# Performance work log

Hardware: AMD Instinct MI355X
Metric: run time of the kernel (lower is better)

Reference implementation:

```python
import jax, jax.numpy as jnp
import numpy as np

N, E, DIN, H, DOUT, G = 100000, 1600000, 32, 64, 8, 64
NUM_PROC = 2
EDGE_DIM = 15


def setup_inputs() -> dict:
    key = jax.random.key(0)
    ks = jax.random.split(key, 20)
    s = 0.1
    return {
        "x": jax.random.normal(ks[0], (N, DIN), dtype=jnp.float32),
        "edge_index": jax.random.randint(ks[1], (2, E), 0, N, dtype=jnp.int32),
        "edge_attr": jax.random.normal(ks[2], (E, EDGE_DIM), dtype=jnp.float32),
        "batch": jnp.sort(jax.random.randint(ks[3], (N,), 0, G, dtype=jnp.int32)),
        "enc_W": jax.random.normal(ks[4], (DIN, H)) * s,
        "enc_b": jnp.zeros((H,), jnp.float32),
        "lin_W": jax.random.normal(ks[5], (NUM_PROC, H, H)) * s,
        "lin_b": jnp.zeros((NUM_PROC, H), jnp.float32),
        "edge_W": jax.random.normal(ks[6], (NUM_PROC, EDGE_DIM, H)) * s,
        "edge_b": jnp.zeros((NUM_PROC, H), jnp.float32),
        "att_W1": jax.random.normal(ks[7], (H, H // 2)) * s,
        "att_b1": jnp.zeros((H // 2,), jnp.float32),
        "att_W2": jax.random.normal(ks[8], (H // 2, 1)) * s,
        "att_b2": jnp.zeros((1,), jnp.float32),
        "dec_W1": jax.random.normal(ks[9], (H, H // 2)) * s,
        "dec_b1": jnp.zeros((H // 2,), jnp.float32),
        "dec_W2": jax.random.normal(ks[10], (H // 2, DOUT)) * s,
        "dec_b2": jnp.zeros((DOUT,), jnp.float32),
    }


def reference(x, edge_index, edge_attr, batch, enc_W, enc_b, lin_W, lin_b,
              edge_W, edge_b, att_W1, att_b1, att_W2, att_b2,
              dec_W1, dec_b1, dec_W2, dec_b2):
    src, dst = edge_index[0], edge_index[1]
    n = x.shape[0]
    # encoder
    h = jax.nn.relu(x @ enc_W + enc_b)
    # message passing layers: gather x_j -> linear + edge embedding -> scatter-add
    for l in range(NUM_PROC):
        msg = h[src] @ lin_W[l] + lin_b[l] + edge_attr @ edge_W[l] + edge_b[l]  # [E, H]
        h = jax.nn.relu(jax.ops.segment_sum(msg, dst, num_segments=n))
    # attention global pooling: segment softmax over graphs in `batch`
    scores = (jax.nn.relu(h @ att_W1 + att_b1) @ att_W2 + att_b2)[:, 0]  # [N]
    m = jax.ops.segment_max(scores, batch, num_segments=G)
    e = jnp.exp(scores - m[batch])
    denom = jax.ops.segment_sum(e, batch, num_segments=G)
    attn = e / denom[batch]
    g = jax.ops.segment_sum(h * attn[:, None], batch, num_segments=G)  # [G, H]
    # decoder
    return jax.nn.relu(g @ dec_W1 + dec_b1) @ dec_W2 + dec_b2
```

## Files before the change

### kernel.cpp

```cpp
#include <hip/hip_runtime.h>

#define DIN 32
#define HDIM 64
#define DOUT 8
#define NGRAPH 64
#define EDIM 15
#define SCAN_BS 512

__device__ __forceinline__ int clampidx(int v, int n) {
    return ((unsigned)v < (unsigned)n) ? v : 0;
}

__device__ __forceinline__ unsigned short f2b(float f) {
    unsigned int u = __float_as_uint(f);
    u = (u + 0x7FFF + ((u >> 16) & 1)) >> 16;
    return (unsigned short)u;
}
__device__ __forceinline__ float b2f(unsigned short b) {
    return __uint_as_float(((unsigned int)b) << 16);
}

__global__ __launch_bounds__(256) void k_zero(float* __restrict__ p, size_t n) {
    size_t i = (size_t)blockIdx.x * blockDim.x + threadIdx.x;
    const size_t stride = (size_t)gridDim.x * blockDim.x;
    for (; i < n; i += stride) p[i] = 0.f;
}

__global__ __launch_bounds__(256) void k_enc_b(const float* __restrict__ x,
                                               const float* __restrict__ W,
                                               const float* __restrict__ b,
                                               unsigned short* __restrict__ h, int n_nodes) {
    __shared__ float xs[4][DIN];
    const int j = threadIdx.x & 63;
    const int q = threadIdx.x >> 6;
    const int n = blockIdx.x * 4 + q;
    const bool ok = (n < n_nodes);
    if (ok && j < DIN) xs[q][j] = x[(size_t)n * DIN + j];
    __syncthreads();
    if (ok) {
        float acc = b[j];
#pragma unroll
        for (int k = 0; k < DIN; ++k) acc = fmaf(xs[q][k], W[k * HDIM + j], acc);
        h[(size_t)n * HDIM + j] = f2b(fmaxf(acc, 0.f));
    }
}

__global__ __launch_bounds__(256) void k_deg(const int* __restrict__ ei,
                                             int* __restrict__ degi,
                                             int* __restrict__ rank, int E, int n_nodes) {
    int e = blockIdx.x * blockDim.x + threadIdx.x;
    if (e < E) rank[e] = atomicAdd(&degi[clampidx(ei[E + e], n_nodes)], 1);
}

__global__ __launch_bounds__(SCAN_BS) void k_blocksum(const int* __restrict__ degi,
                                                      int* __restrict__ bsum, int n) {
    __shared__ int red[SCAN_BS];
    const int t = threadIdx.x;
    const int i = blockIdx.x * SCAN_BS + t;
    red[t] = (i < n) ? degi[i] : 0;
    __syncthreads();
    for (int off = SCAN_BS / 2; off >= 1; off >>= 1) {
        if (t < off) red[t] += red[t + off];
        __syncthreads();
    }
    if (t == 0) bsum[blockIdx.x] = red[0];
}

__global__ __launch_bounds__(64) void k_bscan(const int* __restrict__ bsum,
                                              int* __restrict__ boff,
                                              int* __restrict__ offsets,
                                              int nblk, int n, int E) {
    if (blockIdx.x == 0 && threadIdx.x == 0) {
        int run = 0;
        for (int b = 0; b < nblk; ++b) { boff[b] = run; run += bsum[b]; }
        offsets[n] = E;
    }
}

__global__ __launch_bounds__(64) void k_fillofs(const int* __restrict__ degi,
                                                const int* __restrict__ boff,
                                                int* __restrict__ offsets, int n) {
    if (threadIdx.x != 0) return;
    const int b = blockIdx.x;
    int run = boff[b];
    const int i0 = b * SCAN_BS;
    const int i1 = (i0 + SCAN_BS < n) ? i0 + SCAN_BS : n;
    for (int i = i0; i < i1; ++i) {
        offsets[i] = run;
        run += degi[i];
    }
}

__global__ __launch_bounds__(256) void k_fill(const int* __restrict__ ei,
                                              const int* __restrict__ offsets,
                                              const int* __restrict__ rank,
                                              int2* __restrict__ pe, int E, int n_nodes) {
    int e = blockIdx.x * blockDim.x + threadIdx.x;
    if (e >= E) return;
    int dst = clampidx(ei[E + e], n_nodes);
    int pos = offsets[dst] + rank[e];
    if ((unsigned)pos < (unsigned)E) pe[pos] = make_int2(clampidx(ei[e], n_nodes), e);
}

__global__ __launch_bounds__(256) void k_gxf0(const unsigned short* __restrict__ hprev,
                                              const float* __restrict__ eattr,
                                              const int* __restrict__ degi,
                                              const int* __restrict__ offsets,
                                              const int2* __restrict__ pe,
                                              const float* __restrict__ linW,
                                              const float* __restrict__ linb,
                                              const float* __restrict__ edgeW,
                                              const float* __restrict__ edgeb,
                                              unsigned short* __restrict__ hnext,
                                              float* __restrict__ ea_out,
                                              int n_nodes, int E) {
    __shared__ float As[4][HDIM];
    __shared__ float es[4][EDIM];
    const int j = threadIdx.x & 63;
    const int q = threadIdx.x >> 6;
    const bool ed = (j < EDIM);
    int w  = (blockIdx.x * blockDim.x + threadIdx.x) >> 6;
    const int nw = (gridDim.x * blockDim.x) >> 6;
    for (int n = w; n < n_nodes; n += nw) {
        int rs = offsets[n], re = offsets[n + 1];
        if (rs < 0) rs = 0;
        if (re > E) re = E;
        if (re < rs) re = rs;
        float A0 = 0.f, A1 = 0.f, A2 = 0.f, A3 = 0.f;
        float e0 = 0.f, e1 = 0.f, e2 = 0.f, e3 = 0.f;
        int jj = rs;
        for (; jj + 4 <= re; jj += 4) {
            int2 p0 = pe[jj], p1 = pe[jj + 1], p2 = pe[jj + 2], p3 = pe[jj + 3];
            int s0 = clampidx(p0.x, n_nodes), s1 = clampidx(p1.x, n_nodes);
            int s2 = clampidx(p2.x, n_nodes), s3 = clampidx(p3.x, n_nodes);
            A0 += b2f(hprev[(size_t)s0 * HDIM + j]);
            A1 += b2f(hprev[(size_t)s1 * HDIM + j]);
            A2 += b2f(hprev[(size_t)s2 * HDIM + j]);
            A3 += b2f(hprev[(size_t)s3 * HDIM + j]);
            if (ed) {
                e0 += eattr[(size_t)clampidx(p0.y, E) * EDIM + j];
                e1 += eattr[(size_t)clampidx(p1.y, E) * EDIM + j];
                e2 += eattr[(size_t)clampidx(p2.y, E) * EDIM + j];
                e3 += eattr[(size_t)clampidx(p3.y, E) * EDIM + j];
            }
        }
        for (; jj < re; ++jj) {
            int2 p = pe[jj];
            A0 += b2f(hprev[(size_t)clampidx(p.x, n_nodes) * HDIM + j]);
            if (ed) e0 += eattr[(size_t)clampidx(p.y, E) * EDIM + j];
        }
        As[q][j] = (A0 + A1) + (A2 + A3);
        float eacc = (e0 + e1) + (e2 + e3);
        if (ed) {
            es[q][j] = eacc;
            ea_out[(size_t)n * 16 + j] = eacc;
        }
        __builtin_amdgcn_wave_barrier();
        float acc = (linb[j] + edgeb[j]) * (float)degi[n];
#pragma unroll
        for (int k = 0; k < HDIM; ++k) acc = fmaf(As[q][k], linW[k * HDIM + j], acc);
#pragma unroll
        for (int k = 0; k < EDIM; ++k) acc = fmaf(es[q][k], edgeW[k * HDIM + j], acc);
        hnext[(size_t)n * HDIM + j] = f2b(fmaxf(acc, 0.f));
    }
}

__global__ __launch_bounds__(256) void k_gxf1(const unsigned short* __restrict__ hprev,
                                              const float* __restrict__ ea,
                                              const int* __restrict__ degi,
                                              const int* __restrict__ offsets,
                                              const int2* __restrict__ pe,
                                              const float* __restrict__ linW,
                                              const float* __restrict__ linb,
                                              const float* __restrict__ edgeW,
                                              const float* __restrict__ edgeb,
                                              float* __restrict__ hnext, int n_nodes, int E) {
    __shared__ float As[4][HDIM];
    __shared__ float es[4][EDIM];
    const int j = threadIdx.x & 63;
    const int q = threadIdx.x >> 6;
    int w  = (blockIdx.x * blockDim.x + threadIdx.x) >> 6;
    const int nw = (gridDim.x * blockDim.x) >> 6;
    for (int n = w; n < n_nodes; n += nw) {
        int rs = offsets[n], re = offsets[n + 1];
        if (rs < 0) rs = 0;
        if (re > E) re = E;
        if (re < rs) re = rs;
        float A0 = 0.f, A1 = 0.f, A2 = 0.f, A3 = 0.f;
        int jj = rs;
        for (; jj + 4 <= re; jj += 4) {
            int s0 = clampidx(pe[jj].x,     n_nodes);
            int s1 = clampidx(pe[jj + 1].x, n_nodes);
            int s2 = clampidx(pe[jj + 2].x, n_nodes);
            int s3 = clampidx(pe[jj + 3].x, n_nodes);
            A0 += b2f(hprev[(size_t)s0 * HDIM + j]);
            A1 += b2f(hprev[(size_t)s1 * HDIM + j]);
            A2 += b2f(hprev[(size_t)s2 * HDIM + j]);
            A3 += b2f(hprev[(size_t)s3 * HDIM + j]);
        }
        for (; jj < re; ++jj) A0 += b2f(hprev[(size_t)clampidx(pe[jj].x, n_nodes) * HDIM + j]);
        As[q][j] = (A0 + A1) + (A2 + A3);
        if (j < EDIM) es[q][j] = ea[(size_t)n * 16 + j];
        __builtin_amdgcn_wave_barrier();
        float acc = (linb[j] + edgeb[j]) * (float)degi[n];
#pragma unroll
        for (int k = 0; k < HDIM; ++k) acc = fmaf(As[q][k], linW[k * HDIM + j], acc);
#pragma unroll
        for (int k = 0; k < EDIM; ++k) acc = fmaf(es[q][k], edgeW[k * HDIM + j], acc);
        hnext[(size_t)n * HDIM + j] = fmaxf(acc, 0.f);
    }
}

__global__ __launch_bounds__(256) void k_sc_b(const float* __restrict__ h,
                                              const float* __restrict__ W1,
                                              const float* __restrict__ b1,
                                              const float* __restrict__ W2,
                                              const float* __restrict__ b2,
                                              float* __restrict__ s, int n_nodes) {
    __shared__ float hs[4][HDIM];
    __shared__ double zs[4][32];
    const int j = threadIdx.x & 63;
    const int q = threadIdx.x >> 6;
    const int n = blockIdx.x * 4 + q;
    const bool ok = (n < n_nodes);
    if (ok) hs[q][j] = h[(size_t)n * HDIM + j];
    __syncthreads();
    if (ok && j < 32) {
        double z = (double)b1[j];
#pragma unroll
        for (int k = 0; k < HDIM; ++k) z += (double)hs[q][k] * (double)W1[k * 32 + j];
        if (z < 0.0) z = 0.0;
        zs[q][j] = z * (double)W2[j];
    }
    __syncthreads();
    if (ok && j == 0) {
        double t = (double)b2[0];
        for (int i = 0; i < 32; ++i) t += zs[q][i];
        s[n] = (float)t;
    }
}

__global__ __launch_bounds__(256) void k_pool(const float* __restrict__ s,
                                              const float* __restrict__ h,
                                              const int* __restrict__ batch,
                                              float* __restrict__ g, int n_nodes) {
    const int gi = blockIdx.x;
    __shared__ int se[2];
    __shared__ float redf[256];
    __shared__ double red[256];
    if (threadIdx.x == 0) {
        int lo = 0, hi = n_nodes;
        while (lo < hi) { int mid = (lo + hi) >> 1; if (batch[mid] < gi) lo = mid + 1; else hi = mid; }
        se[0] = lo;
        lo = 0; hi = n_nodes;
        while (lo < hi) { int mid = (lo + hi) >> 1; if (batch[mid] < gi + 1) lo = mid + 1; else hi = mid; }
        se[1] = lo;
    }
    __syncthreads();
    const int start = se[0], end = se[1];
    const int tid = threadIdx.x;

    float mx = -3.4e38f;
    for (int i = start + tid; i < end; i += 256) mx = fmaxf(mx, s[i]);
    redf[tid] = mx;
    __syncthreads();
    for (int off = 128; off >= 1; off >>= 1) {
        if (tid < off) redf[tid] = fmaxf(redf[tid], redf[tid + off]);
        __syncthreads();
    }
    const float m = redf[0];
    __syncthreads();

    double sm = 0.0;
    for (int i = start + tid; i < end; i += 256) sm += exp((double)s[i] - (double)m);
    red[tid] = sm;
    __syncthreads();
    for (int off = 128; off >= 1; off >>= 1) {
        if (tid < off) red[tid] += red[tid + off];
        __syncthreads();
    }
    const double denom = red[0];
    __syncthreads();

    const int d = tid & 63, q = tid >> 6;
    double acc = 0.0;
    for (int i = start + q; i < end; i += 4)
        acc += (double)h[(size_t)i * HDIM + d] * exp((double)s[i] - (double)m);
    red[q * 64 + d] = acc;
    __syncthreads();
    if (tid < 64) {
        double v = red[tid] + red[64 + tid] + red[128 + tid] + red[192 + tid];
        g[gi * HDIM + tid] = (end > start) ? (float)(v / denom) : 0.f;
    }
}

__global__ __launch_bounds__(64) void k_dec_b(const float* __restrict__ g,
                                              const float* __restrict__ W1,
                                              const float* __restrict__ b1,
                                              const float* __restrict__ W2,
                                              const float* __restrict__ b2,
                                              float* __restrict__ out) {
    __shared__ double zs[32];
    const int gi = blockIdx.x;
    const int j = threadIdx.x;
    if (j < 32) {
        double z = (double)b1[j];
#pragma unroll
        for (int k = 0; k < HDIM; ++k) z += (double)g[gi * HDIM + k] * (double)W1[k * 32 + j];
        if (z < 0.0) z = 0.0;
        zs[j] = z;
    }
    __syncthreads();
    if (j < DOUT) {
        double o = (double)b2[j];
#pragma unroll
        for (int i = 0; i < 32; ++i) o += zs[i] * (double)W2[i * DOUT + j];
        out[gi * DOUT + j] = (float)o;
    }
}

extern "C" void kernel_launch(void* const* d_in, const int* in_sizes, int n_in,
                              void* d_out, int out_size, void* d_ws, size_t ws_size,
                              hipStream_t stream) {
    const float* x     = (const float*)d_in[0];
    const int*   ei    = (const int*)d_in[1];
    const float* eattr = (const float*)d_in[2];
    const int*   batch = (const int*)d_in[3];
    const float* encW  = (const float*)d_in[4];
    const float* encb  = (const float*)d_in[5];
    const float* linW  = (const float*)d_in[6];
    const float* linb  = (const float*)d_in[7];
    const float* edgeW = (const float*)d_in[8];
    const float* edgeb = (const float*)d_in[9];
    const float* attW1 = (const float*)d_in[10];
    const float* attb1 = (const float*)d_in[11];
    const float* attW2 = (const float*)d_in[12];
    const float* attb2 = (const float*)d_in[13];
    const float* decW1 = (const float*)d_in[14];
    const float* decb1 = (const float*)d_in[15];
    const float* decW2 = (const float*)d_in[16];
    const float* decb2 = (const float*)d_in[17];

    const int N = in_sizes[0] / DIN;
    const int E = in_sizes[1] / 2;
    const int nblk = (N + SCAN_BS - 1) / SCAN_BS;

    size_t need_bytes = (size_t)N * HDIM * 4
                      + (size_t)N * HDIM * 2 * 2
                      + (size_t)N * 16 * 4
                      + (size_t)N * 4
                      + (size_t)NGRAPH * HDIM * 4
                      + (size_t)E * 8
                      + (size_t)N * 4
                      + (size_t)(N + 2) * 4
                      + (size_t)E * 4
                      + 8192 * 4;
    if (ws_size < need_bytes) {
        return;
    }

    float* B2 = (float*)d_ws;
    unsigned short* hb0 = (unsigned short*)(B2 + (size_t)N * HDIM);
    unsigned short* hb1 = hb0 + (size_t)N * HDIM;
    float* ea = (float*)(hb1 + (size_t)N * HDIM);
    float* sS = ea + (size_t)N * 16;
    float* g  = sS + N;
    int2* pe     = (int2*)(g + NGRAPH * HDIM);
    int* degi    = (int*)(pe + E);
    int* offsets = degi + N;
    int* rank    = offsets + (N + 2);
    int* bsum    = rank + E;
    int* boff    = bsum + 4096;

    k_zero<<<256, 256, 0, stream>>>((float*)degi, (size_t)N);

    k_enc_b<<<(N + 3) / 4, 256, 0, stream>>>(x, encW, encb, hb0, N);
    k_deg<<<(E + 255) / 256, 256, 0, stream>>>(ei, degi, rank, E, N);

    k_blocksum<<<nblk, SCAN_BS, 0, stream>>>(degi, bsum, N);
    k_bscan<<<1, 64, 0, stream>>>(bsum, boff, offsets, nblk, N, E);
    k_fillofs<<<nblk, 64, 0, stream>>>(degi, boff, offsets, N);
    k_fill<<<(E + 255) / 256, 256, 0, stream>>>(ei, offsets, rank, pe, E, N);

    k_gxf0<<<2048, 256, 0, stream>>>(hb0, eattr, degi, offsets, pe,
                                     linW, linb, edgeW, edgeb, hb1, ea, N, E);

    k_gxf1<<<2048, 256, 0, stream>>>(hb1, ea, degi, offsets, pe,
                                     linW + HDIM * HDIM, linb + HDIM,
                                     edgeW + EDIM * HDIM, edgeb + HDIM, B2, N, E);

    k_sc_b<<<(N + 3) / 4, 256, 0, stream>>>(B2, attW1, attb1, attW2, attb2, sS, N);
    k_pool<<<NGRAPH, 256, 0, stream>>>(sS, B2, batch, g, N);
    k_dec_b<<<NGRAPH, 64, 0, stream>>>(g, decW1, decb1, decW2, decb2, (float*)d_out);
}
```

Before: 664.5 us.

## Fuse attention score MLP into second message-passing kernel; nontemporal CSR stores

The attention-score MLP (64->32->1) is now computed inside k_gxf1 right after each node's hidden vector is produced, using shared memory and a wave shuffle reduction, so the separate k_sc_b launch and its re-read of h are removed. The score math moves from double to float precision. The k_deg rank writes and the packed k_fill edge-list writes use nontemporal stores to reduce cache pollution. The fused kernel adds per-node work and register pressure to the gather kernel.

```diff
diff --git a/kernel.cpp b/kernel.cpp
--- a/kernel.cpp
+++ b/kernel.cpp
@@ -49,7 +49,10 @@
                                              int* __restrict__ degi,
                                              int* __restrict__ rank, int E, int n_nodes) {
     int e = blockIdx.x * blockDim.x + threadIdx.x;
-    if (e < E) rank[e] = atomicAdd(&degi[clampidx(ei[E + e], n_nodes)], 1);
+    if (e < E) {
+        int r = atomicAdd(&degi[clampidx(ei[E + e], n_nodes)], 1);
+        __builtin_nontemporal_store(r, &rank[e]);
+    }
 }
 
 __global__ __launch_bounds__(SCAN_BS) void k_blocksum(const int* __restrict__ degi,
@@ -94,12 +97,16 @@
 __global__ __launch_bounds__(256) void k_fill(const int* __restrict__ ei,
                                               const int* __restrict__ offsets,
                                               const int* __restrict__ rank,
-                                              int2* __restrict__ pe, int E, int n_nodes) {
+                                              unsigned long long* __restrict__ pe, int E, int n_nodes) {
     int e = blockIdx.x * blockDim.x + threadIdx.x;
     if (e >= E) return;
     int dst = clampidx(ei[E + e], n_nodes);
     int pos = offsets[dst] + rank[e];
-    if ((unsigned)pos < (unsigned)E) pe[pos] = make_int2(clampidx(ei[e], n_nodes), e);
+    if ((unsigned)pos < (unsigned)E) {
+        unsigned long long packed = (unsigned long long)(unsigned)clampidx(ei[e], n_nodes)
+                                  | ((unsigned long long)(unsigned)e << 32);
+        __builtin_nontemporal_store(packed, &pe[pos]);
+    }
 }
 
 __global__ __launch_bounds__(256) void k_gxf0(const unsigned short* __restrict__ hprev,
@@ -174,8 +181,15 @@
                                               const float* __restrict__ linb,
                                               const float* __restrict__ edgeW,
                                               const float* __restrict__ edgeb,
-                                              float* __restrict__ hnext, int n_nodes, int E) {
+                                              const float* __restrict__ attW1,
+                                              const float* __restrict__ attb1,
+                                              const float* __restrict__ attW2,
+                                              const float* __restrict__ attb2,
+                                              float* __restrict__ hnext,
+                                              float* __restrict__ sOut,
+                                              int n_nodes, int E) {
     __shared__ float As[4][HDIM];
+    __shared__ float hs[4][HDIM];
     __shared__ float es[4][EDIM];
     const int j = threadIdx.x & 63;
     const int q = threadIdx.x >> 6;
@@ -207,36 +221,24 @@
         for (int k = 0; k < HDIM; ++k) acc = fmaf(As[q][k], linW[k * HDIM + j], acc);
 #pragma unroll
         for (int k = 0; k < EDIM; ++k) acc = fmaf(es[q][k], edgeW[k * HDIM + j], acc);
-        hnext[(size_t)n * HDIM + j] = fmaxf(acc, 0.f);
-    }
-}
-
-__global__ __launch_bounds__(256) void k_sc_b(const float* __restrict__ h,
-                                              const float* __restrict__ W1,
-                                              const float* __restrict__ b1,
-                                              const float* __restrict__ W2,
-                                              const float* __restrict__ b2,
-                                              float* __restrict__ s, int n_nodes) {
-    __shared__ float hs[4][HDIM];
-    __shared__ double zs[4][32];
-    const int j = threadIdx.x & 63;
-    const int q = threadIdx.x >> 6;
-    const int n = blockIdx.x * 4 + q;
-    const bool ok = (n < n_nodes);
-    if (ok) hs[q][j] = h[(size_t)n * HDIM + j];
-    __syncthreads();
-    if (ok && j < 32) {
-        double z = (double)b1[j];
-#pragma unroll
-        for (int k = 0; k < HDIM; ++k) z += (double)hs[q][k] * (double)W1[k * 32 + j];
-        if (z < 0.0) z = 0.0;
-        zs[q][j] = z * (double)W2[j];
-    }
-    __syncthreads();
-    if (ok && j == 0) {
-        double t = (double)b2[0];
-        for (int i = 0; i < 32; ++i) t += zs[q][i];
-        s[n] = (float)t;
+        acc = fmaxf(acc, 0.f);
+        hnext[(size_t)n * HDIM + j] = acc;
+        hs[q][j] = acc;
+        __builtin_amdgcn_wave_barrier();
+        float t = 0.f;
+        if (j < 32) {
+            float z = attb1[j];
+#pragma unroll
+            for (int k = 0; k < HDIM; ++k) z = fmaf(hs[q][k], attW1[k * 32 + j], z);
+            t = fmaxf(z, 0.f) * attW2[j];
+        }
+        t += __shfl_xor(t, 1, 64);
+        t += __shfl_xor(t, 2, 64);
+        t += __shfl_xor(t, 4, 64);
+        t += __shfl_xor(t, 8, 64);
+        t += __shfl_xor(t, 16, 64);
+        t += __shfl_xor(t, 32, 64);
+        if (j == 0) sOut[n] = t + attb2[0];
     }
 }
 
@@ -380,16 +382,17 @@
     k_blocksum<<<nblk, SCAN_BS, 0, stream>>>(degi, bsum, N);
     k_bscan<<<1, 64, 0, stream>>>(bsum, boff, offsets, nblk, N, E);
     k_fillofs<<<nblk, 64, 0, stream>>>(degi, boff, offsets, N);
-    k_fill<<<(E + 255) / 256, 256, 0, stream>>>(ei, offsets, rank, pe, E, N);
+    k_fill<<<(E + 255) / 256, 256, 0, stream>>>(ei, offsets, rank,
+                                                (unsigned long long*)pe, E, N);
 
     k_gxf0<<<2048, 256, 0, stream>>>(hb0, eattr, degi, offsets, pe,
                                      linW, linb, edgeW, edgeb, hb1, ea, N, E);
 
     k_gxf1<<<2048, 256, 0, stream>>>(hb1, ea, degi, offsets, pe,
                                      linW + HDIM * HDIM, linb + HDIM,
-                                     edgeW + EDIM * HDIM, edgeb + HDIM, B2, N, E);
-
-    k_sc_b<<<(N + 3) / 4, 256, 0, stream>>>(B2, attW1, attb1, attW2, attb2, sS, N);
+                                     edgeW + EDIM * HDIM, edgeb + HDIM,
+                                     attW1, attb1, attW2, attb2, B2, sS, N, E);
+
     k_pool<<<NGRAPH, 256, 0, stream>>>(sS, B2, batch, g, N);
     k_dec_b<<<NGRAPH, 64, 0, stream>>>(g, decW1, decb1, decW2, decb2, (float*)d_out);
 }
```

Measured after the change: 1.028 ms. 54.6% more time.

## Split attention pooling across chunks with atomics and drop double precision

Applied to the files above, without the earlier changes.

Attention pooling now runs as two kernels over 8 chunks per graph instead of one block per graph. The first kernel finds each graph's max with an order-preserving atomicMax, and the second accumulates exp-weighted sums and denominators with float atomics, caching the weights in shared memory. The score, pooling and decoder kernels switch from double to float math, and the score kernel uses a shuffle reduction instead of a second shared-memory pass. This is meant to fix the poor occupancy of 64 blocks and the slow fp64 exp. In exchange it adds nondeterministic atomic ordering and lower-precision accumulation.

```diff
diff --git a/kernel.cpp b/kernel.cpp
--- a/kernel.cpp
+++ b/kernel.cpp
@@ -20,10 +20,13 @@
     return __uint_as_float(((unsigned int)b) << 16);
 }
 
-__global__ __launch_bounds__(256) void k_zero(float* __restrict__ p, size_t n) {
-    size_t i = (size_t)blockIdx.x * blockDim.x + threadIdx.x;
-    const size_t stride = (size_t)gridDim.x * blockDim.x;
-    for (; i < n; i += stride) p[i] = 0.f;
+__device__ __forceinline__ unsigned int fkey(float f) {
+    unsigned int b = __float_as_uint(f);
+    return (b & 0x80000000u) ? ~b : (b | 0x80000000u);
+}
+__device__ __forceinline__ float funkey(unsigned int k) {
+    unsigned int b = (k & 0x80000000u) ? (k ^ 0x80000000u) : ~k;
+    return __uint_as_float(b);
 }
 
 __global__ __launch_bounds__(256) void k_enc_b(const float* __restrict__ x,
@@ -218,36 +221,34 @@
                                               const float* __restrict__ b2,
                                               float* __restrict__ s, int n_nodes) {
     __shared__ float hs[4][HDIM];
-    __shared__ double zs[4][32];
     const int j = threadIdx.x & 63;
     const int q = threadIdx.x >> 6;
     const int n = blockIdx.x * 4 + q;
     const bool ok = (n < n_nodes);
     if (ok) hs[q][j] = h[(size_t)n * HDIM + j];
-    __syncthreads();
+    __builtin_amdgcn_wave_barrier();
+    float t = 0.f;
     if (ok && j < 32) {
-        double z = (double)b1[j];
-#pragma unroll
-        for (int k = 0; k < HDIM; ++k) z += (double)hs[q][k] * (double)W1[k * 32 + j];
-        if (z < 0.0) z = 0.0;
-        zs[q][j] = z * (double)W2[j];
-    }
-    __syncthreads();
-    if (ok && j == 0) {
-        double t = (double)b2[0];
-        for (int i = 0; i < 32; ++i) t += zs[q][i];
-        s[n] = (float)t;
-    }
-}
-
-__global__ __launch_bounds__(256) void k_pool(const float* __restrict__ s,
-                                              const float* __restrict__ h,
-                                              const int* __restrict__ batch,
-                                              float* __restrict__ g, int n_nodes) {
-    const int gi = blockIdx.x;
+        float z = b1[j];
+#pragma unroll
+        for (int k = 0; k < HDIM; ++k) z = fmaf(hs[q][k], W1[k * 32 + j], z);
+        t = fmaxf(z, 0.f) * W2[j];
+    }
+    t += __shfl_xor(t, 1, 64);
+    t += __shfl_xor(t, 2, 64);
+    t += __shfl_xor(t, 4, 64);
+    t += __shfl_xor(t, 8, 64);
+    t += __shfl_xor(t, 16, 64);
+    if (ok && j == 0) s[n] = t + b2[0];
+}
+
+__global__ __launch_bounds__(256) void k_poolA(const float* __restrict__ s,
+                                               const int* __restrict__ batch,
+                                               unsigned int* __restrict__ gmaxi, int n_nodes) {
+    const int gi = blockIdx.x >> 3;
+    const int c  = blockIdx.x & 7;
     __shared__ int se[2];
-    __shared__ float redf[256];
-    __shared__ double red[256];
+    __shared__ float red[256];
     if (threadIdx.x == 0) {
         int lo = 0, hi = n_nodes;
         while (lo < hi) { int mid = (lo + hi) >> 1; if (batch[mid] < gi) lo = mid + 1; else hi = mid; }
@@ -257,65 +258,94 @@
         se[1] = lo;
     }
     __syncthreads();
-    const int start = se[0], end = se[1];
-    const int tid = threadIdx.x;
-
+    const int start = se[0], len = se[1] - se[0];
+    const int cs = start + (int)(((long long)len * c) >> 3);
+    const int ce = start + (int)(((long long)len * (c + 1)) >> 3);
     float mx = -3.4e38f;
-    for (int i = start + tid; i < end; i += 256) mx = fmaxf(mx, s[i]);
-    redf[tid] = mx;
+    for (int i = cs + threadIdx.x; i < ce; i += 256) mx = fmaxf(mx, s[i]);
+    red[threadIdx.x] = mx;
     __syncthreads();
     for (int off = 128; off >= 1; off >>= 1) {
-        if (tid < off) redf[tid] = fmaxf(redf[tid], redf[tid + off]);
+        if (threadIdx.x < off) red[threadIdx.x] = fmaxf(red[threadIdx.x], red[threadIdx.x + off]);
         __syncthreads();
     }
-    const float m = redf[0];
-    __syncthreads();
-
-    double sm = 0.0;
-    for (int i = start + tid; i < end; i += 256) sm += exp((double)s[i] - (double)m);
-    red[tid] = sm;
+    if (threadIdx.x == 0 && ce > cs) atomicMax(&gmaxi[gi], fkey(red[0]));
+}
+
+__global__ __launch_bounds__(256) void k_poolB(const float* __restrict__ s,
+                                               const float* __restrict__ h,
+                                               const int* __restrict__ batch,
+                                               const unsigned int* __restrict__ gmaxi,
+                                               float* __restrict__ gden,
+                                               float* __restrict__ gacc, int n_nodes) {
+    const int gi = blockIdx.x >> 3;
+    const int c  = blockIdx.x & 7;
+    __shared__ int se[2];
+    __shared__ float ws[256];
+    __shared__ float redd[256];
+    if (threadIdx.x == 0) {
+        int lo = 0, hi = n_nodes;
+        while (lo < hi) { int mid = (lo + hi) >> 1; if (batch[mid] < gi) lo = mid + 1; else hi = mid; }
+        se[0] = lo;
+        lo = 0; hi = n_nodes;
+        while (lo < hi) { int mid = (lo + hi) >> 1; if (batch[mid] < gi + 1) lo = mid + 1; else hi = mid; }
+        se[1] = lo;
+    }
+    __syncthreads();
+    const int start = se[0], len = se[1] - se[0];
+    const int cs = start + (int)(((long long)len * c) >> 3);
+    const int ce = start + (int)(((long long)len * (c + 1)) >> 3);
+    const float m = funkey(gmaxi[gi]);
+    const int tid = threadIdx.x, d = tid & 63, q = tid >> 6;
+    float den = 0.f, acc = 0.f;
+    for (int t0 = cs; t0 < ce; t0 += 256) {
+        const int cnt = (ce - t0 < 256) ? (ce - t0) : 256;
+        __syncthreads();
+        if (tid < cnt) {
+            float wv = __expf(s[t0 + tid] - m);
+            ws[tid] = wv;
+            den += wv;
+        }
+        __syncthreads();
+        for (int i = q; i < cnt; i += 4)
+            acc = fmaf(h[(size_t)(t0 + i) * HDIM + d], ws[i], acc);
+    }
+    redd[tid] = den;
     __syncthreads();
     for (int off = 128; off >= 1; off >>= 1) {
-        if (tid < off) red[tid] += red[tid + off];
+        if (tid < off) redd[tid] += redd[tid + off];
         __syncthreads();
     }
-    const double denom = red[0];
-    __syncthreads();
-
-    const int d = tid & 63, q = tid >> 6;
-    double acc = 0.0;
-    for (int i = start + q; i < end; i += 4)
-        acc += (double)h[(size_t)i * HDIM + d] * exp((double)s[i] - (double)m);
-    red[q * 64 + d] = acc;
-    __syncthreads();
-    if (tid < 64) {
-        double v = red[tid] + red[64 + tid] + red[128 + tid] + red[192 + tid];
-        g[gi * HDIM + tid] = (end > start) ? (float)(v / denom) : 0.f;
-    }
-}
-
-__global__ __launch_bounds__(64) void k_dec_b(const float* __restrict__ g,
+    if (tid == 0 && redd[0] != 0.f) atomicAdd(&gden[gi], redd[0]);
+    if (acc != 0.f) atomicAdd(&gacc[gi * HDIM + d], acc);
+}
+
+__global__ __launch_bounds__(64) void k_dec_b(const float* __restrict__ gacc,
+                                              const float* __restrict__ gden,
                                               const float* __restrict__ W1,
                                               const float* __restrict__ b1,
                                               const float* __restrict__ W2,
                                               const float* __restrict__ b2,
                                               float* __restrict__ out) {
-    __shared__ double zs[32];
+    __shared__ float gg[HDIM];
+    __shared__ float zs[32];
     const int gi = blockIdx.x;
     const int j = threadIdx.x;
+    const float den = gden[gi];
+    gg[j] = (den > 0.f) ? gacc[gi * HDIM + j] / den : 0.f;
+    __syncthreads();
     if (j < 32) {
-        double z = (double)b1[j];
-#pragma unroll
-        for (int k = 0; k < HDIM; ++k) z += (double)g[gi * HDIM + k] * (double)W1[k * 32 + j];
-        if (z < 0.0) z = 0.0;
-        zs[j] = z;
+        float z = b1[j];
+#pragma unroll
+        for (int k = 0; k < HDIM; ++k) z = fmaf(gg[k], W1[k * 32 + j], z);
+        zs[j] = fmaxf(z, 0.f);
     }
     __syncthreads();
     if (j < DOUT) {
-        double o = (double)b2[j];
-#pragma unroll
-        for (int i = 0; i < 32; ++i) o += zs[i] * (double)W2[i * DOUT + j];
-        out[gi * DOUT + j] = (float)o;
+        float o = b2[j];
+#pragma unroll
+        for (int i = 0; i < 32; ++i) o = fmaf(zs[i], W2[i * DOUT + j], o);
+        out[gi * DOUT + j] = o;
     }
 }
 
@@ -349,7 +379,7 @@
                       + (size_t)N * HDIM * 2 * 2
                       + (size_t)N * 16 * 4
                       + (size_t)N * 4
-                      + (size_t)NGRAPH * HDIM * 4
+                      + (size_t)NGRAPH * (HDIM + 2) * 4
                       + (size_t)E * 8
                       + (size_t)N * 4
                       + (size_t)(N + 2) * 4
@@ -364,15 +394,18 @@
     unsigned short* hb1 = hb0 + (size_t)N * HDIM;
     float* ea = (float*)(hb1 + (size_t)N * HDIM);
     float* sS = ea + (size_t)N * 16;
-    float* g  = sS + N;
-    int2* pe     = (int2*)(g + NGRAPH * HDIM);
+    float* gacc = sS + N;
+    float* gden = gacc + NGRAPH * HDIM;
+    unsigned int* gmaxi = (unsigned int*)(gden + NGRAPH);
+    int2* pe     = (int2*)(gmaxi + NGRAPH);
     int* degi    = (int*)(pe + E);
     int* offsets = degi + N;
     int* rank    = offsets + (N + 2);
     int* bsum    = rank + E;
     int* boff    = bsum + 4096;
 
-    k_zero<<<256, 256, 0, stream>>>((float*)degi, (size_t)N);
+    hipMemsetAsync(degi, 0, (size_t)N * sizeof(int), stream);
+    hipMemsetAsync(gacc, 0, (size_t)NGRAPH * (HDIM + 2) * sizeof(float), stream);
 
     k_enc_b<<<(N + 3) / 4, 256, 0, stream>>>(x, encW, encb, hb0, N);
     k_deg<<<(E + 255) / 256, 256, 0, stream>>>(ei, degi, rank, E, N);
@@ -390,6 +423,7 @@
                                      edgeW + EDIM * HDIM, edgeb + HDIM, B2, N, E);
 
     k_sc_b<<<(N + 3) / 4, 256, 0, stream>>>(B2, attW1, attb1, attW2, attb2, sS, N);
-    k_pool<<<NGRAPH, 256, 0, stream>>>(sS, B2, batch, g, N);
-    k_dec_b<<<NGRAPH, 64, 0, stream>>>(g, decW1, decb1, decW2, decb2, (float*)d_out);
-}
+    k_poolA<<<NGRAPH * 8, 256, 0, stream>>>(sS, batch, gmaxi, N);
+    k_poolB<<<NGRAPH * 8, 256, 0, stream>>>(sS, B2, batch, gmaxi, gden, gacc, N);
+    k_dec_b<<<NGRAPH, 64, 0, stream>>>(gacc, gden, decW1, decb1, decW2, decb2, (float*)d_out);
+}
```

New measurement: 567.3 us, median of 2. 14.6% less time.
